# Optimization experiments

Measured on AMD Instinct MI355X. Metric: run time of the kernel, lower is better.

The kernel has to match this reference:

```python
import jax, jax.numpy as jnp
import numpy as np

D, H = 256, 4            # model dim, num heads
HD = D // H              # head dim (even, needed by rotate_half)
B, N, M, NS = 2, 6, 512, 512  # batch, views, t keypoints, s keypoints
EPS = 1e-5


def _linear(x, w, b):
    return x @ w + b


def _ln(x, g, b):
    mu = x.mean(-1, keepdims=True)
    var = ((x - mu) ** 2).mean(-1, keepdims=True)
    return (x - mu) * jax.lax.rsqrt(var + EPS) * g + b


def _ffn(x, f1w, f1b, lng, lnb, f2w, f2b):
    # Linear(2d,2d) -> LayerNorm -> exact GELU -> Linear(2d,d)
    h = jax.nn.gelu(_ln(_linear(x, f1w, f1b), lng, lnb), approximate=False)
    return _linear(h, f2w, f2b)


def _rotate_half(x):
    # pairs (x0,x1) -> (-x1, x0), interleaved
    return jnp.stack((-x[..., 1::2], x[..., 0::2]), axis=-1).reshape(x.shape)


def _rope(freqs, t):
    return t * freqs[0] + _rotate_half(t) * freqs[1]


def _attn(q, k, v):
    sim = jnp.einsum('...id,...jd->...ij', q, k) * (q.shape[-1] ** -0.5)
    return jnp.einsum('...ij,...jd->...id', jax.nn.softmax(sim, axis=-1), v)


def _self_block(x, enc, qkv_w, qkv_b, out_w, out_b, *ffn_p):
    b, n_img, m, d = x.shape
    enc = jnp.swapaxes(enc, 2, 3)  # encoding.dim()==6 path
    qkv = _linear(x, qkv_w, qkv_b).reshape(b, n_img, m, H, HD, 3)
    qkv = jnp.swapaxes(qkv, -4, -3)  # [b,N,H,m,hd,3]
    q, k, v = qkv[..., 0], qkv[..., 1], qkv[..., 2]
    ctx = _attn(_rope(enc, q), _rope(enc, k), v)  # [b,N,H,m,hd]
    msg = _linear(jnp.swapaxes(ctx, -3, -2).reshape(b, n_img, m, d), out_w, out_b)
    return x + _ffn(jnp.concatenate([x, msg], -1), *ffn_p)


def _t2t_block(t, qkv_w, qkv_b, out_w, out_b, *ffn_p):
    t2 = jnp.swapaxes(t, 1, 2)  # [b,m,N,d]
    b, m, n_img, d = t2.shape
    qkv = _linear(t2, qkv_w, qkv_b).reshape(b, m, n_img, H, HD, 3)
    qkv = jnp.swapaxes(qkv, 3, 2)  # [b,m,H,N,hd,3]
    q, k, v = qkv[..., 0], qkv[..., 1], qkv[..., 2]
    ctx = _attn(q, k, v)  # [b,m,H,N,hd]
    msg = _linear(jnp.swapaxes(ctx, 3, 2).reshape(b, m, n_img, d), out_w, out_b)
    return jnp.swapaxes(t2 + _ffn(jnp.concatenate([t2, msg], -1), *ffn_p), 1, 2)


def _s2s_block(s, q_enc, k_enc, qkv_w, qkv_b, out_w, out_b, *ffn_p):
    b, n_img, n, d = s.shape
    qkv = _linear(s, qkv_w, qkv_b).reshape(b, n_img, n, H, HD, 3)
    qkv = jnp.swapaxes(jnp.swapaxes(qkv, -4, -3), -5, -4)  # [b,H,N,n,hd,3]
    q, k, v = qkv[..., 0], qkv[..., 1], qkv[..., 2]
    # expand queries across all views, RoPE per (i,j) view pair
    q = jnp.broadcast_to(q[:, :, None], (b, H, n_img, n_img, n, HD))
    q = _rope(q_enc, q).reshape(b, H, n_img, n_img * n, HD)
    k = _rope(k_enc, k)
    ctx = _attn(q, k, v).reshape(b, H, n_img, n_img, n, HD)
    # drop diagonal (i==j) entries exactly like boolean-mask indexing in torch
    off = np.nonzero(~np.eye(n_img, dtype=bool).ravel())[0]
    ctx = ctx.reshape(b, H, n_img * n_img, n, HD)[:, :, off]
    ctx = ctx.reshape(b, H, n_img - 1, n_img, n, HD).mean(2)  # [b,H,N,n,hd]
    ctx = jnp.swapaxes(jnp.swapaxes(ctx, 1, 2), 2, 3).reshape(b, n_img, n, d)
    msg = _linear(ctx, out_w, out_b)
    return s + _ffn(jnp.concatenate([s, msg], -1), *ffn_p)


def _cross_block(d0, d1, q_w, q_b, kv_w, kv_b, out_w, out_b, *ffn_p):
    b, n_img, m, d = d0.shape
    m1 = d1.shape[2]
    q = jnp.swapaxes(_linear(d0, q_w, q_b).reshape(b, n_img, m, H, HD), 2, 3)
    kv = jnp.swapaxes(_linear(d1, kv_w, kv_b).reshape(b, n_img, m1, H, HD, 2), 2, 3)
    ctx = _attn(q, kv[..., 0], kv[..., 1])  # [b,N,H,m,hd]
    msg = _linear(jnp.swapaxes(ctx, 2, 3).reshape(b, n_img, m, d), out_w, out_b)
    return d0 + _ffn(jnp.concatenate([d0, msg], -1), *ffn_p)


def setup_inputs() -> dict:
    key = jax.random.key(0)
    ks = iter(jax.random.split(key, 80))
    f32 = jnp.float32

    def lin(din, dout):
        return (jax.random.normal(next(ks), (din, dout), f32) * (din ** -0.5),
                jnp.zeros((dout,), f32))

    inp = {}
    inp['t_desc'] = jax.random.normal(next(ks), (B, N, M, D), f32)
    inp['s_desc'] = jax.random.normal(next(ks), (B, N, NS, D), f32)
    inp['t_encoding'] = jax.random.normal(next(ks), (2, 1, 1, N, M, HD), f32)
    inp['s_encoding'] = jax.random.normal(next(ks), (2, 1, 1, N, NS, HD), f32)
    inp['q_encoding'] = jax.random.normal(next(ks), (2, 1, 1, N, N, 1, HD), f32)
    inp['k_encoding'] = jax.random.normal(next(ks), (2, 1, 1, N, NS, HD), f32)
    for pre in ('sa', 'ss', 'tt'):
        inp[pre + '_qkv_w'], inp[pre + '_qkv_b'] = lin(D, 3 * D)
        inp[pre + '_out_w'], inp[pre + '_out_b'] = lin(D, D)
        inp[pre + '_f1_w'], inp[pre + '_f1_b'] = lin(2 * D, 2 * D)
        inp[pre + '_ln_g'] = jnp.ones((2 * D,), f32)
        inp[pre + '_ln_b'] = jnp.zeros((2 * D,), f32)
        inp[pre + '_f2_w'], inp[pre + '_f2_b'] = lin(2 * D, D)
    inp['ca_q_w'], inp['ca_q_b'] = lin(D, D)
    inp['ca_kv_w'], inp['ca_kv_b'] = lin(D, 2 * D)
    inp['ca_out_w'], inp['ca_out_b'] = lin(D, D)
    inp['ca_f1_w'], inp['ca_f1_b'] = lin(2 * D, 2 * D)
    inp['ca_ln_g'] = jnp.ones((2 * D,), f32)
    inp['ca_ln_b'] = jnp.zeros((2 * D,), f32)
    inp['ca_f2_w'], inp['ca_f2_b'] = lin(2 * D, D)
    inp['cf_w1'], inp['cf_b1'] = lin(D, D)
    inp['cf_w2'], inp['cf_b2'] = lin(D, 1)
    return inp


def reference(t_desc, s_desc, t_encoding, s_encoding, q_encoding, k_encoding,
              sa_qkv_w, sa_qkv_b, sa_out_w, sa_out_b, sa_f1_w, sa_f1_b, sa_ln_g, sa_ln_b, sa_f2_w, sa_f2_b,
              ss_qkv_w, ss_qkv_b, ss_out_w, ss_out_b, ss_f1_w, ss_f1_b, ss_ln_g, ss_ln_b, ss_f2_w, ss_f2_b,
              tt_qkv_w, tt_qkv_b, tt_out_w, tt_out_b, tt_f1_w, tt_f1_b, tt_ln_g, tt_ln_b, tt_f2_w, tt_f2_b,
              ca_q_w, ca_q_b, ca_kv_w, ca_kv_b, ca_out_w, ca_out_b, ca_f1_w, ca_f1_b, ca_ln_g, ca_ln_b, ca_f2_w, ca_f2_b,
              cf_w1, cf_b1, cf_w2, cf_b2):
    sa = (sa_qkv_w, sa_qkv_b, sa_out_w, sa_out_b, sa_f1_w, sa_f1_b, sa_ln_g, sa_ln_b, sa_f2_w, sa_f2_b)
    t = _self_block(t_desc, t_encoding, *sa)   # shared SelfBlock weights
    s = _self_block(s_desc, s_encoding, *sa)
    t = _t2t_block(t, tt_qkv_w, tt_qkv_b, tt_out_w, tt_out_b, tt_f1_w, tt_f1_b, tt_ln_g, tt_ln_b, tt_f2_w, tt_f2_b)
    s = _s2s_block(s, q_encoding, k_encoding, ss_qkv_w, ss_qkv_b, ss_out_w, ss_out_b, ss_f1_w, ss_f1_b, ss_ln_g, ss_ln_b, ss_f2_w, ss_f2_b)
    ca = (ca_q_w, ca_q_b, ca_kv_w, ca_kv_b, ca_out_w, ca_out_b, ca_f1_w, ca_f1_b, ca_ln_g, ca_ln_b, ca_f2_w, ca_f2_b)
    t2 = _cross_block(t, s, *ca)               # shared CrossBlock weights
    s2 = _cross_block(s, t, *ca)
    conf = _linear(jax.nn.relu(_linear(jax.lax.stop_gradient(s), cf_w1, cf_b1)), cf_w2, cf_b2)[..., 0]
    return t2, s2, conf
```

## Files before the change

kernel.cpp:

```cpp
#include <hip/hip_runtime.h>
#include <hip/hip_bf16.h>
#include <math.h>

constexpr int kD   = 256;
constexpr int kH   = 4;
constexpr int kHD  = 64;
constexpr int kB   = 2;
constexpr int kN   = 6;
constexpr int kM   = 512;
constexpr int kRowsH = kB*kN*kM;
constexpr int kRows  = 2*kRowsH;
constexpr int kGrpH  = kB*kN*kH;
constexpr int kGrp   = 2*kGrpH;
constexpr size_t kTOK = (size_t)kRowsH*kD;
constexpr size_t kEncSlab = (size_t)kN*kM*kHD;
constexpr size_t kQEncSlab = (size_t)kN*kN*kHD;
constexpr float kL2E = 1.4426950408889634f;

typedef unsigned short u16;
typedef __attribute__((ext_vector_type(8))) short s16x8;
typedef __attribute__((ext_vector_type(4))) float f32x4;

__device__ __forceinline__ float wred_sum(float v){
  #pragma unroll
  for (int m=32;m>0;m>>=1) v += __shfl_xor(v, m, 64);
  return v;
}
__device__ __forceinline__ u16 f2b(float x){
  union { float f; unsigned u; } a; a.f = x;
  unsigned r = a.u + 0x7fffu + ((a.u >> 16) & 1u);
  return (u16)(r >> 16);
// ... 55 lines not shown
      C[(size_t)(row0+ty*4+i)*512 + col0+tx*4+j] = acc[i][j];
}

__global__ __launch_bounds__(256) void biasfuse_k(FuseArgs fa)
{
  const int set = blockIdx.x >> 1;
  const int n = (blockIdx.x & 1)*256 + threadIdx.x;
  const float* W1 = fa.W1[set];
  const float* bo = fa.bout[set];
  float s = fa.b1[set][n];
  for (int k = 0; k < 256; ++k)
    s = fmaf(bo[k], W1[(size_t)(256+k)*512 + n], s);
  fa.b1p[set*512 + n] = s;
}

struct WtDesc { const float* W; const float* W2; u16* Wt; int K; int N; int ntiles; };
struct WtTable { WtDesc d[18]; };

__global__ __launch_bounds__(256) void wtcast_k(WtTable tab)
{
  int t = blockIdx.x, mi = 0;
  while (t >= tab.d[mi].ntiles) { t -= tab.d[mi].ntiles; ++mi; }
  const float* W = tab.d[mi].W;
  const float* W2 = tab.d[mi].W2;
  u16* Wt = tab.d[mi].Wt;
  const int K = tab.d[mi].K, N = tab.d[mi].N;
  const int ktn = K >> 5;
  const int nt = t / ktn, kt = t % ktn;
  const int n0 = nt*128, k0 = kt*32;
  u16* dst = Wt + (size_t)t*4096;
  #pragma unroll
  for (int s = 0; s < 2; ++s) {
    const int idx0 = (s*256 + (int)threadIdx.x)*8;
    const int ar = idx0 >> 5;
    const int w8 = (idx0 >> 3) & 3;
    const int sw = (ar >> 1) & 3;
    int kk = k0 + ((w8 ^ sw) << 3);
    const int n  = n0 + ar;
    const float* src = W;
    if (W2 && kk >= 256) { src = W2; kk -= 256; }
    union { u16 u[8]; s16x8 v; } o;
    #pragma unroll
    for (int e = 0; e < 8; ++e)
      o.u[e] = f2b(src[(size_t)(kk + e)*N + n]);
    *(s16x8*)(dst + idx0) = o.v;
  }
}

template<bool A1B, bool A2B, bool CB>
__global__ __launch_bounds__(256) void mmad_k(
    const void* __restrict__ A1a, const void* __restrict__ A1b,
    const void* __restrict__ A2a, const void* __restrict__ A2b, int K1,
    const u16* __restrict__ Wa, const u16* __restrict__ Wb,
    const float* __restrict__ bia, const float* __restrict__ bib,
    const float* __restrict__ bi2a, const float* __restrict__ bi2b, int Ns,
    const float* __restrict__ Ra, const float* __restrict__ Rb,
    void* __restrict__ Cp, int N, int K, int Mh, int doRelu)
{
  __shared__ u16 As[128*32];
  __shared__ u16 Bs[128*32];
  const int tid = threadIdx.x;
  const int lane = tid & 63, w = tid >> 6;
  const int gx = gridDim.x;
  const int nblk = gx * gridDim.y;
  int flat = blockIdx.y*gx + blockIdx.x;
  if (!(nblk & 7)) flat = (flat & 7)*(nblk >> 3) + (flat >> 3);
  const int bxx = flat % gx, byy = flat / gx;
  const int row0 = byy*128, col0 = bxx*128;
  const bool sec = (row0 >= Mh);
  const int lr0 = sec ? row0 - Mh : row0;
  const void* A1 = sec ? A1b : A1a;
  const void* A2 = sec ? A2b : A2a;
// ... 59 lines not shown
    }
    #pragma unroll
    for (int fn = 0; fn < 4; ++fn) {
      const int c = wc + fn*16 + (lane & 15);
      const int g = (lane >> 4) ^ ((c >> 1) & 3);
      bfv[fn] = *(const s16x8*)(&Bs[c*32 + g*8]);
    }
    #pragma unroll
    for (int fm = 0; fm < 4; ++fm)
      #pragma unroll
      for (int fn = 0; fn < 4; ++fn)
        acc[fm][fn] = __builtin_amdgcn_mfma_f32_16x16x32_bf16(af[fm], bfv[fn], acc[fm][fn], 0, 0, 0);
    __syncthreads();
  }

  #pragma unroll
  for (int fm = 0; fm < 4; ++fm) {
    const int ro = wr + fm*16 + (lane >> 4)*4;
    #pragma unroll
    for (int fn = 0; fn < 4; ++fn) {
      const int cc = col0 + wc + fn*16 + (lane & 15);
      const float bv = (cc < Ns) ? bias[cc] : bias2[cc - Ns];
      #pragma unroll
      for (int j = 0; j < 4; ++j) {
        float v = acc[fm][fn][j] + bv;
        if (R) v += R[(size_t)(lr0 + ro + j)*N + cc];
        if (doRelu) v = fmaxf(v, 0.f);
        const size_t idx = (size_t)(row0 + ro + j)*N + cc;
        if constexpr (CB) ((u16*)Cp)[idx] = f2b(v);
        else              ((float*)Cp)[idx] = v;
      }
    }
  }
}

__global__ __launch_bounds__(256) void prep_self_k(
    const u16* __restrict__ qkvU, const float* __restrict__ t_enc,
    const float* __restrict__ s_enc,
    u16* __restrict__ Qb, u16* __restrict__ Kb, u16* __restrict__ Vt)
{
  __shared__ u16 vs[64][66];
  const int g = blockIdx.x >> 3, i0 = (blockIdx.x & 7)*64;
  const int h = g & 3, bn = g >> 2;
  const float* enc = (bn < 12) ? t_enc : s_enc;
  const int n = (bn < 12 ? bn : bn - 12) % kN;
  const int c = threadIdx.x & 63, t4 = threadIdx.x >> 6;
  const float sgn = (c & 1) ? 1.f : -1.f;
  #pragma unroll 4
  for (int rr = 0; rr < 16; ++rr) {
    const int il = rr*4 + t4, i = i0 + il;
    const u16* base = qkvU + ((size_t)bn*kM + i)*768 + h*192;
    const float q = b2f(base[c*3]), k = b2f(base[c*3+1]);
    const float qp = b2f(base[(c^1)*3]), kp = b2f(base[(c^1)*3+1]);
    const size_t eo = ((size_t)(n*kM + i))*kHD + c;
    const float e0 = enc[eo], e1 = enc[kEncSlab + eo];
    Qb[((size_t)g*kM + i)*kHD + c] = f2b((q*e0 + sgn*qp*e1)*0.125f);
    Kb[((size_t)g*kM + i)*kHD + c] = f2b(k*e0 + sgn*kp*e1);
    vs[il][c] = base[c*3+2];
  }
  __syncthreads();
  #pragma unroll 4
  for (int rr = 0; rr < 16; ++rr) {
    const int cc = rr*4 + t4;
    Vt[((size_t)g*kHD + cc)*kM + i0 + c] = vs[c][cc];
  }
}

__global__ __launch_bounds__(256) void prep_s2s_k(
    const u16* __restrict__ qkvU, const float* __restrict__ kenc,
    float* __restrict__ Qs, u16* __restrict__ Kb, u16* __restrict__ Vt)
{
  __shared__ u16 vs[64][66];
  const int g = blockIdx.x >> 3, i0 = (blockIdx.x & 7)*64;
  const int view = g % kN, bh = g / kN;
  const int h = bh & 3, b = bh >> 2;
  const int c = threadIdx.x & 63, t4 = threadIdx.x >> 6;
  const float sgn = (c & 1) ? 1.f : -1.f;
  #pragma unroll 4
  for (int rr = 0; rr < 16; ++rr) {
    const int il = rr*4 + t4, i = i0 + il;
    const u16* base = qkvU + ((size_t)(kRowsH + (b*kN+view)*kM + i))*768 + h*192;
    const float k = b2f(base[c*3+1]), kp = b2f(base[(c^1)*3+1]);
    const size_t eo = ((size_t)(view*kM + i))*kHD + c;
    const float e0 = kenc[eo], e1 = kenc[kEncSlab + eo];
    Qs[((size_t)g*kM + i)*kHD + c] = b2f(base[c*3]);
    Kb[((size_t)g*kM + i)*kHD + c] = f2b(k*e0 + sgn*kp*e1);
    vs[il][c] = base[c*3+2];
  }
  __syncthreads();
  #pragma unroll 4
  for (int rr = 0; rr < 16; ++rr) {
    const int cc = rr*4 + t4;
    Vt[((size_t)g*kHD + cc)*kM + i0 + c] = vs[c][cc];
  }
}

__global__ __launch_bounds__(256) void prep_cross_k(
    const u16* __restrict__ qkvC, u16* __restrict__ Kb, u16* __restrict__ Vt)
{
  __shared__ u16 vs[64][66];
  const int g = blockIdx.x >> 3, i0 = (blockIdx.x & 7)*64;
  const int h = g & 3, bn = g >> 2;
  const int src = (bn < 12) ? bn + 12 : bn - 12;
  const int c = threadIdx.x & 63, t4 = threadIdx.x >> 6;
  #pragma unroll 4
  for (int rr = 0; rr < 16; ++rr) {
    const int il = rr*4 + t4, i = i0 + il;
    const u16* base = qkvC + ((size_t)src*kM + i)*768 + 256 + h*128;
    Kb[((size_t)g*kM + i)*kHD + c] = f2b(b2f(base[c*2]) * 0.125f);
    vs[il][c] = base[c*2+1];
  }
  __syncthreads();
  #pragma unroll 4
  for (int rr = 0; rr < 16; ++rr) {
    const int cc = rr*4 + t4;
    Vt[((size_t)g*kHD + cc)*kM + i0 + c] = vs[c][cc];
  }
}

template<int CROSSQ>
__global__ __launch_bounds__(256) void attn_mm_k(
    const u16* __restrict__ Qb, const u16* __restrict__ Kb,
    const u16* __restrict__ Vt, u16* __restrict__ ctx)
{
  const int w = threadIdx.x >> 6, lane = threadIdx.x & 63;
  const int bij = (blockIdx.x & 7)*48 + (blockIdx.x >> 3);
  const int g = bij >> 2, qblk = bij & 3;
  const int h = g & 3, bn = g >> 2;
  const int q0 = qblk*128 + w*32;
  const int qr = lane & 15, hi = lane >> 4;
  const bool subhi = (hi & 1), up = (hi >= 2);

  s16x8 qf0[2], qf1[2];
  #pragma unroll
  for (int f = 0; f < 2; ++f) {
    const u16* qp = CROSSQ
      ? Qb + ((size_t)(bn*kM + q0 + f*16 + qr))*768 + h*kHD + hi*8
      : Qb + ((size_t)g*kM + q0 + f*16 + qr)*kHD + hi*8;
    qf0[f] = *(const s16x8*)(qp);
    qf1[f] = *(const s16x8*)(qp + 32);
  }

  const u16* Kg = Kb + (size_t)g*kM*kHD;
  const u16* Vg = Vt + (size_t)g*kHD*kM;
  f32x4 acc[2][4] = {};
  float m[2] = {-1e30f, -1e30f}, l[2] = {0.f, 0.f};

  for (int kc = 0; kc < 16; ++kc) {
    const int k0 = kc*32;
    s16x8 a0[2], a1[2];
    #pragma unroll
    for (int t = 0; t < 2; ++t) {
      const u16* kp = Kg + ((size_t)(k0 + t*16 + qr))*kHD + hi*8;
      a0[t] = *(const s16x8*)(kp);
      a1[t] = *(const s16x8*)(kp + 32);
    }
    s16x8 pa[2];
    #pragma unroll
    for (int f = 0; f < 2; ++f) {
// ... 63 lines not shown
    lf += __shfl_xor(lf, 16); lf += __shfl_xor(lf, 32);
    const float li = 1.f/lf;
    const float l0 = __shfl(li, hi*4+0), l1 = __shfl(li, hi*4+1);
    const float l2 = __shfl(li, hi*4+2), l3 = __shfl(li, hi*4+3);
    #pragma unroll
    for (int db = 0; db < 4; ++db) {
      const size_t base = ((size_t)(bn*kM + q0 + f*16 + hi*4))*kD + h*kHD + db*16 + qr;
      ctx[base + 0*kD] = f2b(acc[f][db][0]*l0);
      ctx[base + 1*kD] = f2b(acc[f][db][1]*l1);
      ctx[base + 2*kD] = f2b(acc[f][db][2]*l2);
      ctx[base + 3*kD] = f2b(acc[f][db][3]*l3);
    }
  }
}

__device__ __forceinline__ void rope4(const f32x4 x, const f32x4 e0, const f32x4 e1, float o[4])
{
  o[0] = x[0]*e0[0] - x[1]*e1[0];
  o[1] = x[1]*e0[1] + x[0]*e1[1];
  o[2] = x[2]*e0[2] - x[3]*e1[2];
  o[3] = x[3]*e0[3] + x[2]*e1[3];
}

__global__ __launch_bounds__(256) void attn_s2s_k(
    const float* __restrict__ Qraw, const u16* __restrict__ Kb,
    const u16* __restrict__ Vt, const float* __restrict__ qenc,
    u16* __restrict__ ctx5)
{
  const int w = threadIdx.x >> 6, lane = threadIdx.x & 63;
  const int bij = (blockIdx.x & 7)*120 + (blockIdx.x >> 3);
  const int bh = bij / 120;
  const int rest = bij % 120;
  const int col = rest / 20;
  const int rem = rest % 20;
  const int qblk = rem / 5, split = rem % 5;
  const int q0 = qblk*128 + w*32;
  const int qr = lane & 15, hi = lane >> 4;
  const bool subhi = (hi & 1), up = (hi >= 2);

  const int e  = split*6 + col;
  const int iv = e/5;
  const int j0 = e%5;
  const int jv = j0 + (j0 >= iv ? 1 : 0);

  s16x8 qf0[2], qf1[2];
  #pragma unroll
  for (int f = 0; f < 2; ++f) {
    const float* qp = Qraw + ((size_t)(bh*kN + jv)*kM + q0 + f*16 + qr)*kHD + hi*8;
    const float* ep = qenc + ((size_t)(iv*kN + jv))*kHD + hi*8;
    union { u16 u[8]; s16x8 v; } A, B;
    float o[4];
    rope4(*(const f32x4*)(qp),   *(const f32x4*)(ep),   *(const f32x4*)(ep+kQEncSlab), o);
    #pragma unroll
    for (int j = 0; j < 4; ++j) A.u[j] = f2b(o[j]*0.125f);
    rope4(*(const f32x4*)(qp+4), *(const f32x4*)(ep+4), *(const f32x4*)(ep+kQEncSlab+4), o);
    #pragma unroll
    for (int j = 0; j < 4; ++j) A.u[4+j] = f2b(o[j]*0.125f);
    rope4(*(const f32x4*)(qp+32), *(const f32x4*)(ep+32), *(const f32x4*)(ep+kQEncSlab+32), o);
    #pragma unroll
    for (int j = 0; j < 4; ++j) B.u[j] = f2b(o[j]*0.125f);
    rope4(*(const f32x4*)(qp+36), *(const f32x4*)(ep+36), *(const f32x4*)(ep+kQEncSlab+36), o);
    #pragma unroll
    for (int j = 0; j < 4; ++j) B.u[4+j] = f2b(o[j]*0.125f);
    qf0[f] = A.v; qf1[f] = B.v;
  }

  const int g2 = bh*kN + iv;
  const u16* Kg = Kb + (size_t)g2*kM*kHD;
  const u16* Vg = Vt + (size_t)g2*kHD*kM;
  f32x4 acc[2][4] = {};
  float m[2] = {-1e30f, -1e30f}, l[2] = {0.f, 0.f};

  for (int kc = 0; kc < 16; ++kc) {
    const int k0 = kc*32;
    s16x8 a0[2], a1[2];
    #pragma unroll
    for (int t = 0; t < 2; ++t) {
      const u16* kp = Kg + ((size_t)(k0 + t*16 + qr))*kHD + hi*8;
      a0[t] = *(const s16x8*)(kp);
      a1[t] = *(const s16x8*)(kp + 32);
    }
    s16x8 pa[2];
    #pragma unroll
    for (int f = 0; f < 2; ++f) {
// ... 82 lines not shown
{
  const size_t i4 = ((size_t)blockIdx.x*256 + threadIdx.x)*4;
  float s0=0.f, s1=0.f, s2=0.f, s3=0.f;
  #pragma unroll
  for (int sp = 0; sp < 5; ++sp) {
    uint2 d = *(const uint2*)(c5 + sp*kTOK + i4);
    s0 += b2f((u16)(d.x & 0xffff)); s1 += b2f((u16)(d.x >> 16));
    s2 += b2f((u16)(d.y & 0xffff)); s3 += b2f((u16)(d.y >> 16));
  }
  union { u16 u[4]; uint2 d; } o;
  o.u[0]=f2b(s0); o.u[1]=f2b(s1); o.u[2]=f2b(s2); o.u[3]=f2b(s3);
  *(uint2*)(outU + i4) = o.d;
}

__global__ __launch_bounds__(256) void attn_t2t_k(
    const u16* __restrict__ qkvU, u16* __restrict__ ctxU)
{
  const int wid = blockIdx.x*4 + (threadIdx.x >> 6);
  const int lane = threadIdx.x & 63;
  const int m = wid & 511;
  const int t = wid >> 9;
  const int nq = t % kN;
  const int bh = t / kN;
  const int h = bh & 3, b = bh >> 2;
  const u16* pb[kN];
  #pragma unroll
  for (int nk = 0; nk < kN; ++nk)
    pb[nk] = qkvU + ((size_t)(b*kN+nk)*kM + m)*768 + h*192;
  const float qc = b2f(pb[nq][lane*3]);
  float sim[kN];
  #pragma unroll
  for (int nk = 0; nk < kN; ++nk)
    sim[nk] = wred_sum(qc * b2f(pb[nk][lane*3+1])) * 0.125f;
  float mx = sim[0];
  #pragma unroll
  for (int nk = 1; nk < kN; ++nk) mx = fmaxf(mx, sim[nk]);
  float p[kN], s = 0.f;
  #pragma unroll
  for (int nk = 0; nk < kN; ++nk) { p[nk] = expf(sim[nk]-mx); s += p[nk]; }
  const float inv = 1.f/s;
  float o = 0.f;
  #pragma unroll
  for (int nk = 0; nk < kN; ++nk) o = fmaf(p[nk], b2f(pb[nk][lane*3+2]), o);
  ctxU[((size_t)(b*kN+nq)*kM + m)*kD + h*kHD + lane] = f2b(o*inv);
}

__global__ __launch_bounds__(256) void lngelu_k(
    const float* __restrict__ x, u16* __restrict__ y,
    const float* __restrict__ g0, const float* __restrict__ b0,
    const float* __restrict__ g1, const float* __restrict__ b1, int Mh)
{
  const int row = blockIdx.x;
  const int tid = threadIdx.x;
  const float* g = (row < Mh) ? g0 : g1;
  const float* bb = (row < Mh) ? b0 : b1;
  const float* xr = x + (size_t)row*512;
  const float v0 = xr[tid], v1 = xr[tid+256];
  const int w = tid >> 6, lane = tid & 63;
// ... 35 lines not shown
  const float* s_enc  = F(3);
  const float* q_enc  = F(4);
  const float* k_enc  = F(5);

  char* base = (char*)d_ws;
  float* xts = (float*)base;
  float* xt = xts;
  float* xs = xts + kTOK;
  char* R1  = base + 2*kTOK*sizeof(float);
  char* CTX = R1 + 4*kTOK*sizeof(float);
  char* MSG = CTX + 2*kTOK*sizeof(u16);
  u16* Qb16 = (u16*)(MSG + kTOK*sizeof(float));
  u16* Kb16 = Qb16 + 2*kTOK;
  u16* Vt16 = Kb16 + 2*kTOK;
  u16* wsW  = Vt16 + 2*kTOK;
  u16*   qkvU  = (u16*)R1;
  float* hbuf  = (float*)R1;
  u16*   ctx5  = (u16*)R1;
  float* Wtmp  = (float*)R1;
  u16*   ctxU  = (u16*)CTX;
  float* Qs2s  = (float*)MSG;
  float* confb = (float*)MSG;
  u16*   yU    = (u16*)CTX;

  float* out_t2s2 = (float*)d_out;
  float* out_conf = (float*)d_out + 2*kTOK;

  WtTable tab;
  int nd = 0, total_tiles = 0;
  size_t woff = 0;
  const u16* wp[18];
  auto addw = [&](int idx, const float* W2, int K, int N){
    u16* dst = wsW + woff;
    tab.d[nd] = { F(idx), W2, dst, K, N, (N>>7)*(K>>5) };
    total_tiles += tab.d[nd].ntiles;
    wp[nd] = dst;
    woff += (size_t)K*N;
    ++nd;
    return nd-1;
  };
  const int W_SA_QKV = addw(6,  nullptr, 256, 768);
  const int W_SA_F1  = addw(10, Wtmp + 0*131072, 512, 512);
  const int W_SA_F2  = addw(14, nullptr, 512, 256);
  const int W_SS_QKV = addw(16, nullptr, 256, 768);
  const int W_SS_F1  = addw(20, Wtmp + 1*131072, 512, 512);
  const int W_SS_F2  = addw(24, nullptr, 512, 256);
  const int W_TT_QKV = addw(26, nullptr, 256, 768);
  const int W_TT_F1  = addw(30, Wtmp + 2*131072, 512, 512);
  const int W_TT_F2  = addw(34, nullptr, 512, 256);
  const int W_CA_Q   = addw(36, nullptr, 256, 256);
  const int W_CA_KV  = addw(38, nullptr, 256, 512);
  const int W_CA_F1  = addw(42, Wtmp + 3*131072, 512, 512);
  const int W_CA_F2  = addw(46, nullptr, 512, 256);
  const int W_CF_1   = addw(48, nullptr, 256, 256);
  (void)W_CA_KV;
  float* b1p = (float*)(wsW + woff);

  FuseArgs fa;
  fa.Wout[0]=F(8);  fa.Wout[1]=F(18); fa.Wout[2]=F(28); fa.Wout[3]=F(40);
  fa.W1[0]=F(10);   fa.W1[1]=F(20);   fa.W1[2]=F(30);   fa.W1[3]=F(42);
  fa.bout[0]=F(9);  fa.bout[1]=F(19); fa.bout[2]=F(29); fa.bout[3]=F(41);
  fa.b1[0]=F(11);   fa.b1[1]=F(21);   fa.b1[2]=F(31);   fa.b1[3]=F(43);
  fa.Wtmp = Wtmp; fa.b1p = b1p;
  wfuse_k<<<128, 256, 0, stream>>>(fa);
  biasfuse_k<<<8, 256, 0, stream>>>(fa);
  wtcast_k<<<total_tiles, 256, 0, stream>>>(tab);

  auto mm_f32_to_b16 = [&](const float* a1a, const float* a1b, int wa, int wb2,
                           const float* ba, const float* bb2, u16* c, int N_, int K_){
    dim3 grid(N_/128, kRows/128);
    mmad_k<false,false,true><<<grid,256,0,stream>>>(a1a, a1b, nullptr, nullptr, K_,
        wp[wa], wp[wb2], ba, bb2, ba, bb2, N_, nullptr, nullptr, c, N_, K_, kRowsH, 0);
  };
  auto mm_f1 = [&](const float* a1a, const float* a1b, const u16* a2a, const u16* a2b,
                   int wa, int wb2, const float* ba, const float* bb2, float* c){
    dim3 grid(512/128, kRows/128);
    mmad_k<false,true,false><<<grid,256,0,stream>>>(a1a, a1b, a2a, a2b, 256,
        wp[wa], wp[wb2], ba, bb2, ba, bb2, 512, nullptr, nullptr, c, 512, 512, kRowsH, 0);
  };
  auto mm_f2 = [&](const u16* a1a, const u16* a1b, int wa, int wb2,
                   const float* ba, const float* bb2,
                   const float* ra, const float* rb, float* c){
    dim3 grid(256/128, kRows/128);
    mmad_k<true,false,false><<<grid,256,0,stream>>>(a1a, a1b, nullptr, nullptr, 512,
        wp[wa], wp[wb2], ba, bb2, ba, bb2, 256, ra, rb, c, 256, 512, kRowsH, 0);
  };

  mm_f32_to_b16(t_desc, s_desc, W_SA_QKV, W_SA_QKV, F(7), F(7), qkvU, 768, 256);
  prep_self_k<<<kGrp*8, 256, 0, stream>>>(qkvU, t_enc, s_enc, Qb16, Kb16, Vt16);
  attn_mm_k<0><<<384, 256, 0, stream>>>(Qb16, Kb16, Vt16, ctxU);
  mm_f1(t_desc, s_desc, ctxU, ctxU + kTOK, W_SA_F1, W_SA_F1, b1p+0*512, b1p+0*512, hbuf);
  lngelu_k<<<kRows, 256, 0, stream>>>(hbuf, yU, F(12), F(13), F(12), F(13), kRowsH);
  mm_f2(yU, yU + (size_t)kRowsH*512, W_SA_F2, W_SA_F2, F(15), F(15), t_desc, s_desc, xts);

  mm_f32_to_b16(xt, xs, W_TT_QKV, W_SS_QKV, F(27), F(17), qkvU, 768, 256);
  prep_s2s_k<<<kGrpH*8, 256, 0, stream>>>(qkvU, k_enc, Qs2s, Kb16, Vt16);
  attn_t2t_k<<<(kB*kH*kN*kM)/4, 256, 0, stream>>>(qkvU, ctxU);
  attn_s2s_k<<<960, 256, 0, stream>>>(Qs2s, Kb16, Vt16, q_enc, ctx5);
  sum5_k<<<(int)(kTOK/1024), 256, 0, stream>>>(ctx5, ctxU + kTOK);
  mm_f1(xt, xs, ctxU, ctxU + kTOK, W_TT_F1, W_SS_F1, b1p+2*512, b1p+1*512, hbuf);
  lngelu_k<<<kRows, 256, 0, stream>>>(hbuf, yU, F(32), F(33), F(22), F(23), kRowsH);
  mm_f2(yU, yU + (size_t)kRowsH*512, W_TT_F2, W_SS_F2, F(35), F(25), xt, xs, xts);

  {
    dim3 grid(2, kRowsH/128);
    mmad_k<false,false,false><<<grid,256,0,stream>>>(xs, xs, nullptr, nullptr, 256,
        wp[W_CF_1], wp[W_CF_1], F(49), F(49), F(49), F(49), 256,
        nullptr, nullptr, confb, 256, 256, kRowsH, 1);
  }
  conf_dot_k<<<kRowsH/4, 256, 0, stream>>>(confb, F(50), F(51), out_conf);

  {
    dim3 grid(768/128, kRows/128);
    mmad_k<false,false,true><<<grid,256,0,stream>>>(xt, xs, nullptr, nullptr, 256,
        wp[W_CA_Q], wp[W_CA_Q], F(37), F(37), F(39), F(39), 256,
        nullptr, nullptr, qkvU, 768, 256, kRowsH, 0);
  }
  prep_cross_k<<<kGrp*8, 256, 0, stream>>>(qkvU, Kb16, Vt16);
  attn_mm_k<1><<<384, 256, 0, stream>>>(qkvU, Kb16, Vt16, ctxU);
  mm_f1(xt, xs, ctxU, ctxU + kTOK, W_CA_F1, W_CA_F1, b1p+3*512, b1p+3*512, hbuf);
  lngelu_k<<<kRows, 256, 0, stream>>>(hbuf, yU, F(44), F(45), F(44), F(45), kRowsH);
  mm_f2(yU, yU + (size_t)kRowsH*512, W_CA_F2, W_CA_F2, F(47), F(47), xt, xs, out_t2s2);
}
```

Baseline: 483.6 us.

## Fuse QKV projection epilogues with RoPE and head-major scatter, drop prep kernels

The QKV weight columns are permuted at cast time so each output tile groups q, k and v for a head. The GEMM epilogue then applies the bias, RoPE (exchanging the pair partner via a lane shuffle) and the scaling, and writes Q/K/V directly in per-head layouts. This removes the intermediate qkv buffer and the separate prep kernels. A small transpose kernel still builds V^T, and t2t and s2s attention now read the pre-split buffers, at the cost of scattered 2-byte stores from the GEMM epilogue.

Measured after the change: 508.2 us. 1.05x slower.

```diff
diff --git a/kernel.cpp b/kernel.cpp
--- a/kernel.cpp
+++ b/kernel.cpp
@@ -15,6 +15,7 @@
 constexpr size_t kTOK = (size_t)kRowsH*kD;
 constexpr size_t kEncSlab = (size_t)kN*kM*kHD;
 constexpr size_t kQEncSlab = (size_t)kN*kN*kHD;
+constexpr size_t kGS = (size_t)kM*kHD;
 constexpr float kL2E = 1.4426950408889634f;
 
 typedef unsigned short u16;
@@ -100,8 +101,8 @@
   fa.b1p[set*512 + n] = s;
 }
 
-struct WtDesc { const float* W; const float* W2; u16* Wt; int K; int N; int ntiles; };
-struct WtTable { WtDesc d[18]; };
+struct WtDesc { const float* W; const float* W2; u16* Wt; int K; int N; int ntiles; int perm; };
+struct WtTable { WtDesc d[16]; };
 
 __global__ __launch_bounds__(256) void wtcast_k(WtTable tab)
 {
@@ -110,7 +111,7 @@
   const float* W = tab.d[mi].W;
   const float* W2 = tab.d[mi].W2;
   u16* Wt = tab.d[mi].Wt;
-  const int K = tab.d[mi].K, N = tab.d[mi].N;
+  const int K = tab.d[mi].K, N = tab.d[mi].N, perm = tab.d[mi].perm;
   const int ktn = K >> 5;
   const int nt = t / ktn, kt = t % ktn;
   const int n0 = nt*128, k0 = kt*32;
@@ -123,17 +124,30 @@
     const int sw = (ar >> 1) & 3;
     int kk = k0 + ((w8 ^ sw) << 3);
     const int n  = n0 + ar;
+    int o = n;
+    if (perm == 1) {
+      const int hh = n / 192, rem = n % 192;
+      o = hh*192 + (rem & 63)*3 + (rem >> 6);
+    } else if (perm == 2) {
+      const int hh = n >> 7, rem = n & 127;
+      o = hh*128 + (rem & 63)*2 + (rem >> 6);
+    }
     const float* src = W;
     if (W2 && kk >= 256) { src = W2; kk -= 256; }
-    union { u16 u[8]; s16x8 v; } o;
+    union { u16 u[8]; s16x8 v; } ov;
     #pragma unroll
     for (int e = 0; e < 8; ++e)
-      o.u[e] = f2b(src[(size_t)(kk + e)*N + n]);
-    *(s16x8*)(dst + idx0) = o.v;
-  }
-}
-
-template<bool A1B, bool A2B, bool CB>
+      ov.u[e] = f2b(src[(size_t)(kk + e)*N + o]);
+    *(s16x8*)(dst + idx0) = ov.v;
+  }
+}
+
+struct EpiArgs {
+  const float* enc_t; const float* enc_s;
+  u16 *Qb, *Kb, *Vst, *Qs2s;
+};
+
+template<bool A1B, bool A2B, int EPI>
 __global__ __launch_bounds__(256) void mmad_k(
     const void* __restrict__ A1a, const void* __restrict__ A1b,
     const void* __restrict__ A2a, const void* __restrict__ A2b, int K1,
@@ -141,7 +155,7 @@
     const float* __restrict__ bia, const float* __restrict__ bib,
     const float* __restrict__ bi2a, const float* __restrict__ bi2b, int Ns,
     const float* __restrict__ Ra, const float* __restrict__ Rb,
-    void* __restrict__ Cp, int N, int K, int Mh, int doRelu)
+    float* __restrict__ Cp, int N, int K, int Mh, int doRelu, EpiArgs ea)
 {
   __shared__ u16 As[128*32];
   __shared__ u16 Bs[128*32];
@@ -231,111 +245,129 @@
     __syncthreads();
   }
 
-  #pragma unroll
-  for (int fm = 0; fm < 4; ++fm) {
-    const int ro = wr + fm*16 + (lane >> 4)*4;
-    #pragma unroll
-    for (int fn = 0; fn < 4; ++fn) {
-      const int cc = col0 + wc + fn*16 + (lane & 15);
-      const float bv = (cc < Ns) ? bias[cc] : bias2[cc - Ns];
-      #pragma unroll
-      for (int j = 0; j < 4; ++j) {
-        float v = acc[fm][fn][j] + bv;
-        if (R) v += R[(size_t)(lr0 + ro + j)*N + cc];
-        if (doRelu) v = fmaxf(v, 0.f);
-        const size_t idx = (size_t)(row0 + ro + j)*N + cc;
-        if constexpr (CB) ((u16*)Cp)[idx] = f2b(v);
-        else              ((float*)Cp)[idx] = v;
+  if constexpr (EPI == 0) {
+    #pragma unroll
+    for (int fm = 0; fm < 4; ++fm) {
+      const int ro = wr + fm*16 + (lane >> 4)*4;
+      #pragma unroll
+      for (int fn = 0; fn < 4; ++fn) {
+        const int cc = col0 + wc + fn*16 + (lane & 15);
+        const float bv = (cc < Ns) ? bias[cc] : bias2[cc - Ns];
+        #pragma unroll
+        for (int j = 0; j < 4; ++j) {
+          float v = acc[fm][fn][j] + bv;
+          if (R) v += R[(size_t)(lr0 + ro + j)*N + cc];
+          if (doRelu) v = fmaxf(v, 0.f);
+          Cp[(size_t)(row0 + ro + j)*N + cc] = v;
+        }
       }
     }
-  }
-}
-
-__global__ __launch_bounds__(256) void prep_self_k(
-    const u16* __restrict__ qkvU, const float* __restrict__ t_enc,
-    const float* __restrict__ s_enc,
-    u16* __restrict__ Qb, u16* __restrict__ Kb, u16* __restrict__ Vt)
+  } else {
+    const int bn = row0 >> 9;
+    const int ib = (row0 & 511);
+    #pragma unroll
+    for (int fm = 0; fm < 4; ++fm) {
+      const int ro = wr + fm*16 + (lane >> 4)*4;
+      #pragma unroll
+      for (int fn = 0; fn < 4; ++fn) {
+        const int cc = col0 + wc + fn*16 + (lane & 15);
+        if constexpr (EPI == 1 || EPI == 2) {
+          const int hh = cc/192, rem = cc%192;
+          const int which = rem >> 6, hd = rem & 63;
+          const float bv = bias[hh*192 + hd*3 + which];
+          const float sgn = (hd & 1) ? 1.f : -1.f;
+          #pragma unroll
+          for (int j = 0; j < 4; ++j) {
+            const int i = ib + ro + j;
+            const float vb = acc[fm][fn][j] + bv;
+            if constexpr (EPI == 1) {
+              const bool isT = (bn < 12);
+              const float* enc = isT ? ea.enc_t : ea.enc_s;
+              const int n = (isT ? bn : bn - 12) % kN;
+              const size_t base = ((size_t)(bn*4+hh)*kM + i)*kHD + hd;
+              if (which == 2) {
+                ea.Vst[base] = f2b(vb);
+              } else {
+                const float vp = __shfl_xor(vb, 1);
+                const size_t eo = ((size_t)(n*kM + i))*kHD + hd;
+                const float rv = vb*enc[eo] + sgn*vp*enc[kEncSlab + eo];
+                if (which == 0) ea.Qb[base] = f2b(rv*0.125f);
+                else            ea.Kb[base] = f2b(rv);
+              }
+            } else {
+              if (bn < 12) {
+                const size_t base = ((size_t)(bn*4+hh)*kM + i)*kHD + hd;
+                if (which == 0)      ea.Qb [base] = f2b(vb);
+                else if (which == 1) ea.Kb [48*kGS + base] = f2b(vb);
+                else                 ea.Vst[48*kGS + base] = f2b(vb);
+              } else {
+                const int bns = bn - 12;
+                const int b = bns / kN, view = bns % kN;
+                const int g2 = (b*4 + hh)*kN + view;
+                const size_t base = ((size_t)g2*kM + i)*kHD + hd;
+                if (which == 0) {
+                  ea.Qs2s[base] = f2b(vb*0.125f);
+                } else if (which == 1) {
+                  const float vp = __shfl_xor(vb, 1);
+                  const size_t eo = ((size_t)(view*kM + i))*kHD + hd;
+                  const float rv = vb*ea.enc_s[eo] + sgn*vp*ea.enc_s[kEncSlab + eo];
+                  ea.Kb[base] = f2b(rv);
+                } else {
+                  ea.Qb[48*kGS + base] = f2b(vb);
+                }
+              }
+            }
+          }
+        } else {
+          if (cc < 256) {
+            const int hh = cc >> 6, hd = cc & 63;
+            const float bv = bias[cc];
+            #pragma unroll
+            for (int j = 0; j < 4; ++j) {
+              const int i = ib + ro + j;
+              const float vb = acc[fm][fn][j] + bv;
+              ea.Qb[((size_t)(bn*4+hh)*kM + i)*kHD + hd] = f2b(vb*0.125f);
+            }
+          } else {
+            const int p = cc - 256;
+            const int hh = p >> 7, rem = p & 127;
+            const int which = rem >> 6, hd = rem & 63;
+            const float bv = bias2[hh*128 + hd*2 + which];
+            const int bnsw = (bn < 12) ? bn + 12 : bn - 12;
+            #pragma unroll
+            for (int j = 0; j < 4; ++j) {
+              const int i = ib + ro + j;
+              const float vb = acc[fm][fn][j] + bv;
+              const size_t base = ((size_t)(bnsw*4+hh)*kM + i)*kHD + hd;
+              if (which == 0) ea.Kb [base] = f2b(vb);
+              else            ea.Vst[base] = f2b(vb);
+            }
+          }
+        }
+      }
+    }
+  }
+}
+
+__global__ __launch_bounds__(256) void vtrans_k(const u16* __restrict__ src,
+                                               u16* __restrict__ dst)
 {
   __shared__ u16 vs[64][66];
   const int g = blockIdx.x >> 3, i0 = (blockIdx.x & 7)*64;
-  const int h = g & 3, bn = g >> 2;
-  const float* enc = (bn < 12) ? t_enc : s_enc;
-  const int n = (bn < 12 ? bn : bn - 12) % kN;
   const int c = threadIdx.x & 63, t4 = threadIdx.x >> 6;
-  const float sgn = (c & 1) ? 1.f : -1.f;
   #pragma unroll 4
   for (int rr = 0; rr < 16; ++rr) {
-    const int il = rr*4 + t4, i = i0 + il;
-    const u16* base = qkvU + ((size_t)bn*kM + i)*768 + h*192;
-    const float q = b2f(base[c*3]), k = b2f(base[c*3+1]);
-    const float qp = b2f(base[(c^1)*3]), kp = b2f(base[(c^1)*3+1]);
-    const size_t eo = ((size_t)(n*kM + i))*kHD + c;
-    const float e0 = enc[eo], e1 = enc[kEncSlab + eo];
-    Qb[((size_t)g*kM + i)*kHD + c] = f2b((q*e0 + sgn*qp*e1)*0.125f);
-    Kb[((size_t)g*kM + i)*kHD + c] = f2b(k*e0 + sgn*kp*e1);
-    vs[il][c] = base[c*3+2];
+    const int il = rr*4 + t4;
+    vs[il][c] = src[((size_t)g*kM + i0 + il)*kHD + c];
   }
   __syncthreads();
   #pragma unroll 4
   for (int rr = 0; rr < 16; ++rr) {
     const int cc = rr*4 + t4;
-    Vt[((size_t)g*kHD + cc)*kM + i0 + c] = vs[c][cc];
-  }
-}
-
-__global__ __launch_bounds__(256) void prep_s2s_k(
-    const u16* __restrict__ qkvU, const float* __restrict__ kenc,
-    float* __restrict__ Qs, u16* __restrict__ Kb, u16* __restrict__ Vt)
-{
-  __shared__ u16 vs[64][66];
-  const int g = blockIdx.x >> 3, i0 = (blockIdx.x & 7)*64;
-  const int view = g % kN, bh = g / kN;
-  const int h = bh & 3, b = bh >> 2;
-  const int c = threadIdx.x & 63, t4 = threadIdx.x >> 6;
-  const float sgn = (c & 1) ? 1.f : -1.f;
-  #pragma unroll 4
-  for (int rr = 0; rr < 16; ++rr) {
-    const int il = rr*4 + t4, i = i0 + il;
-    const u16* base = qkvU + ((size_t)(kRowsH + (b*kN+view)*kM + i))*768 + h*192;
-    const float k = b2f(base[c*3+1]), kp = b2f(base[(c^1)*3+1]);
-    const size_t eo = ((size_t)(view*kM + i))*kHD + c;
-    const float e0 = kenc[eo], e1 = kenc[kEncSlab + eo];
-    Qs[((size_t)g*kM + i)*kHD + c] = b2f(base[c*3]);
-    Kb[((size_t)g*kM + i)*kHD + c] = f2b(k*e0 + sgn*kp*e1);
-    vs[il][c] = base[c*3+2];
-  }
-  __syncthreads();
-  #pragma unroll 4
-  for (int rr = 0; rr < 16; ++rr) {
-    const int cc = rr*4 + t4;
-    Vt[((size_t)g*kHD + cc)*kM + i0 + c] = vs[c][cc];
-  }
-}
-
-__global__ __launch_bounds__(256) void prep_cross_k(
-    const u16* __restrict__ qkvC, u16* __restrict__ Kb, u16* __restrict__ Vt)
-{
-  __shared__ u16 vs[64][66];
-  const int g = blockIdx.x >> 3, i0 = (blockIdx.x & 7)*64;
-  const int h = g & 3, bn = g >> 2;
-  const int src = (bn < 12) ? bn + 12 : bn - 12;
-  const int c = threadIdx.x & 63, t4 = threadIdx.x >> 6;
-  #pragma unroll 4
-  for (int rr = 0; rr < 16; ++rr) {
-    const int il = rr*4 + t4, i = i0 + il;
-    const u16* base = qkvC + ((size_t)src*kM + i)*768 + 256 + h*128;
-    Kb[((size_t)g*kM + i)*kHD + c] = f2b(b2f(base[c*2]) * 0.125f);
-    vs[il][c] = base[c*2+1];
-  }
-  __syncthreads();
-  #pragma unroll 4
-  for (int rr = 0; rr < 16; ++rr) {
-    const int cc = rr*4 + t4;
-    Vt[((size_t)g*kHD + cc)*kM + i0 + c] = vs[c][cc];
-  }
-}
-
-template<int CROSSQ>
+    dst[((size_t)g*kHD + cc)*kM + i0 + c] = vs[c][cc];
+  }
+}
+
 __global__ __launch_bounds__(256) void attn_mm_k(
     const u16* __restrict__ Qb, const u16* __restrict__ Kb,
     const u16* __restrict__ Vt, u16* __restrict__ ctx)
@@ -351,15 +383,13 @@
   s16x8 qf0[2], qf1[2];
   #pragma unroll
   for (int f = 0; f < 2; ++f) {
-    const u16* qp = CROSSQ
-      ? Qb + ((size_t)(bn*kM + q0 + f*16 + qr))*768 + h*kHD + hi*8
-      : Qb + ((size_t)g*kM + q0 + f*16 + qr)*kHD + hi*8;
+    const u16* qp = Qb + ((size_t)g*kM + q0 + f*16 + qr)*kHD + hi*8;
     qf0[f] = *(const s16x8*)(qp);
     qf1[f] = *(const s16x8*)(qp + 32);
   }
 
-  const u16* Kg = Kb + (size_t)g*kM*kHD;
-  const u16* Vg = Vt + (size_t)g*kHD*kM;
+  const u16* Kg = Kb + (size_t)g*kGS;
+  const u16* Vg = Vt + (size_t)g*kGS;
   f32x4 acc[2][4] = {};
   float m[2] = {-1e30f, -1e30f}, l[2] = {0.f, 0.f};
 
@@ -453,16 +483,20 @@
   }
 }
 
-__device__ __forceinline__ void rope4(const f32x4 x, const f32x4 e0, const f32x4 e1, float o[4])
-{
-  o[0] = x[0]*e0[0] - x[1]*e1[0];
-  o[1] = x[1]*e0[1] + x[0]*e1[1];
-  o[2] = x[2]*e0[2] - x[3]*e1[2];
-  o[3] = x[3]*e0[3] + x[2]*e1[3];
+__device__ __forceinline__ s16x8 ropeq(const u16* qp, const float* ep)
+{
+  union { u16 u[8]; s16x8 v; } o;
+  #pragma unroll
+  for (int u2 = 0; u2 < 8; u2 += 2) {
+    const float a = b2f(qp[u2]), b = b2f(qp[u2+1]);
+    o.u[u2]   = f2b(a*ep[u2]   - b*ep[kQEncSlab + u2]);
+    o.u[u2+1] = f2b(b*ep[u2+1] + a*ep[kQEncSlab + u2+1]);
+  }
+  return o.v;
 }
 
 __global__ __launch_bounds__(256) void attn_s2s_k(
-    const float* __restrict__ Qraw, const u16* __restrict__ Kb,
+    const u16* __restrict__ Qs2sU, const u16* __restrict__ Kb,
     const u16* __restrict__ Vt, const float* __restrict__ qenc,
     u16* __restrict__ ctx5)
 {
@@ -483,30 +517,17 @@
   const int jv = j0 + (j0 >= iv ? 1 : 0);
 
   s16x8 qf0[2], qf1[2];
+  const float* ep = qenc + ((size_t)(iv*kN + jv))*kHD + hi*8;
   #pragma unroll
   for (int f = 0; f < 2; ++f) {
-    const float* qp = Qraw + ((size_t)(bh*kN + jv)*kM + q0 + f*16 + qr)*kHD + hi*8;
-    const float* ep = qenc + ((size_t)(iv*kN + jv))*kHD + hi*8;
-    union { u16 u[8]; s16x8 v; } A, B;
-    float o[4];
-    rope4(*(const f32x4*)(qp),   *(const f32x4*)(ep),   *(const f32x4*)(ep+kQEncSlab), o);
-    #pragma unroll
-    for (int j = 0; j < 4; ++j) A.u[j] = f2b(o[j]*0.125f);
-    rope4(*(const f32x4*)(qp+4), *(const f32x4*)(ep+4), *(const f32x4*)(ep+kQEncSlab+4), o);
-    #pragma unroll
-    for (int j = 0; j < 4; ++j) A.u[4+j] = f2b(o[j]*0.125f);
-    rope4(*(const f32x4*)(qp+32), *(const f32x4*)(ep+32), *(const f32x4*)(ep+kQEncSlab+32), o);
-    #pragma unroll
-    for (int j = 0; j < 4; ++j) B.u[j] = f2b(o[j]*0.125f);
-    rope4(*(const f32x4*)(qp+36), *(const f32x4*)(ep+36), *(const f32x4*)(ep+kQEncSlab+36), o);
-    #pragma unroll
-    for (int j = 0; j < 4; ++j) B.u[4+j] = f2b(o[j]*0.125f);
-    qf0[f] = A.v; qf1[f] = B.v;
+    const u16* qp = Qs2sU + ((size_t)(bh*kN + jv)*kM + q0 + f*16 + qr)*kHD + hi*8;
+    qf0[f] = ropeq(qp, ep);
+    qf1[f] = ropeq(qp + 32, ep + 32);
   }
 
   const int g2 = bh*kN + iv;
-  const u16* Kg = Kb + (size_t)g2*kM*kHD;
-  const u16* Vg = Vt + (size_t)g2*kHD*kM;
+  const u16* Kg = Kb + (size_t)g2*kGS;
+  const u16* Vg = Vt + (size_t)g2*kGS;
   f32x4 acc[2][4] = {};
   float m[2] = {-1e30f, -1e30f}, l[2] = {0.f, 0.f};
 
@@ -619,7 +640,8 @@
 }
 
 __global__ __launch_bounds__(256) void attn_t2t_k(
-    const u16* __restrict__ qkvU, u16* __restrict__ ctxU)
+    const u16* __restrict__ Qp, const u16* __restrict__ Kp,
+    const u16* __restrict__ Vp, u16* __restrict__ ctxU)
 {
   const int wid = blockIdx.x*4 + (threadIdx.x >> 6);
   const int lane = threadIdx.x & 63;
@@ -628,15 +650,13 @@
   const int nq = t % kN;
   const int bh = t / kN;
   const int h = bh & 3, b = bh >> 2;
-  const u16* pb[kN];
-  #pragma unroll
-  for (int nk = 0; nk < kN; ++nk)
-    pb[nk] = qkvU + ((size_t)(b*kN+nk)*kM + m)*768 + h*192;
-  const float qc = b2f(pb[nq][lane*3]);
+  const float qc = b2f(Qp[((size_t)((b*kN+nq)*4+h)*kM + m)*kHD + lane]);
   float sim[kN];
   #pragma unroll
-  for (int nk = 0; nk < kN; ++nk)
-    sim[nk] = wred_sum(qc * b2f(pb[nk][lane*3+1])) * 0.125f;
+  for (int nk = 0; nk < kN; ++nk) {
+    const size_t gb = ((size_t)((b*kN+nk)*4+h)*kM + m)*kHD + lane;
+    sim[nk] = wred_sum(qc * b2f(Kp[gb])) * 0.125f;
+  }
   float mx = sim[0];
   #pragma unroll
   for (int nk = 1; nk < kN; ++nk) mx = fmaxf(mx, sim[nk]);
@@ -646,7 +666,10 @@
   const float inv = 1.f/s;
   float o = 0.f;
   #pragma unroll
-  for (int nk = 0; nk < kN; ++nk) o = fmaf(p[nk], b2f(pb[nk][lane*3+2]), o);
+  for (int nk = 0; nk < kN; ++nk) {
+    const size_t gb = ((size_t)((b*kN+nk)*4+h)*kM + m)*kHD + lane;
+    o = fmaf(p[nk], b2f(Vp[gb]), o);
+  }
   ctxU[((size_t)(b*kN+nq)*kM + m)*kD + h*kHD + lane] = f2b(o*inv);
 }
 
@@ -712,12 +735,12 @@
   u16* Kb16 = Qb16 + 2*kTOK;
   u16* Vt16 = Kb16 + 2*kTOK;
   u16* wsW  = Vt16 + 2*kTOK;
-  u16*   qkvU  = (u16*)R1;
   float* hbuf  = (float*)R1;
   u16*   ctx5  = (u16*)R1;
   float* Wtmp  = (float*)R1;
   u16*   ctxU  = (u16*)CTX;
-  float* Qs2s  = (float*)MSG;
+  u16*   vstg  = (u16*)MSG;
+  u16*   Qs2sU = (u16*)MSG;
   float* confb = (float*)MSG;
   u16*   yU    = (u16*)CTX;
 
@@ -727,30 +750,30 @@
   WtTable tab;
   int nd = 0, total_tiles = 0;
   size_t woff = 0;
-  const u16* wp[18];
-  auto addw = [&](int idx, const float* W2, int K, int N){
+  const u16* wp[16];
+  auto addw = [&](int idx, const float* W2, int K, int N, int perm){
     u16* dst = wsW + woff;
-    tab.d[nd] = { F(idx), W2, dst, K, N, (N>>7)*(K>>5) };
+    tab.d[nd] = { F(idx), W2, dst, K, N, (N>>7)*(K>>5), perm };
     total_tiles += tab.d[nd].ntiles;
     wp[nd] = dst;
     woff += (size_t)K*N;
     ++nd;
     return nd-1;
   };
-  const int W_SA_QKV = addw(6,  nullptr, 256, 768);
-  const int W_SA_F1  = addw(10, Wtmp + 0*131072, 512, 512);
-  const int W_SA_F2  = addw(14, nullptr, 512, 256);
-  const int W_SS_QKV = addw(16, nullptr, 256, 768);
-  const int W_SS_F1  = addw(20, Wtmp + 1*131072, 512, 512);
-  const int W_SS_F2  = addw(24, nullptr, 512, 256);
-  const int W_TT_QKV = addw(26, nullptr, 256, 768);
-  const int W_TT_F1  = addw(30, Wtmp + 2*131072, 512, 512);
-  const int W_TT_F2  = addw(34, nullptr, 512, 256);
-  const int W_CA_Q   = addw(36, nullptr, 256, 256);
-  const int W_CA_KV  = addw(38, nullptr, 256, 512);
-  const int W_CA_F1  = addw(42, Wtmp + 3*131072, 512, 512);
-  const int W_CA_F2  = addw(46, nullptr, 512, 256);
-  const int W_CF_1   = addw(48, nullptr, 256, 256);
+  const int W_SA_QKV = addw(6,  nullptr, 256, 768, 1);
+  const int W_SA_F1  = addw(10, Wtmp + 0*131072, 512, 512, 0);
+  const int W_SA_F2  = addw(14, nullptr, 512, 256, 0);
+  const int W_SS_QKV = addw(16, nullptr, 256, 768, 1);
+  const int W_SS_F1  = addw(20, Wtmp + 1*131072, 512, 512, 0);
+  const int W_SS_F2  = addw(24, nullptr, 512, 256, 0);
+  const int W_TT_QKV = addw(26, nullptr, 256, 768, 1);
+  const int W_TT_F1  = addw(30, Wtmp + 2*131072, 512, 512, 0);
+  const int W_TT_F2  = addw(34, nullptr, 512, 256, 0);
+  const int W_CA_Q   = addw(36, nullptr, 256, 256, 0);
+  const int W_CA_KV  = addw(38, nullptr, 256, 512, 2);
+  const int W_CA_F1  = addw(42, Wtmp + 3*131072, 512, 512, 0);
+  const int W_CA_F2  = addw(46, nullptr, 512, 256, 0);
+  const int W_CF_1   = addw(48, nullptr, 256, 256, 0);
   (void)W_CA_KV;
   float* b1p = (float*)(wsW + woff);
 
@@ -764,37 +787,44 @@
   biasfuse_k<<<8, 256, 0, stream>>>(fa);
   wtcast_k<<<total_tiles, 256, 0, stream>>>(tab);
 
-  auto mm_f32_to_b16 = [&](const float* a1a, const float* a1b, int wa, int wb2,
-                           const float* ba, const float* bb2, u16* c, int N_, int K_){
-    dim3 grid(N_/128, kRows/128);
-    mmad_k<false,false,true><<<grid,256,0,stream>>>(a1a, a1b, nullptr, nullptr, K_,
-        wp[wa], wp[wb2], ba, bb2, ba, bb2, N_, nullptr, nullptr, c, N_, K_, kRowsH, 0);
-  };
+  const EpiArgs ea0 = {};
   auto mm_f1 = [&](const float* a1a, const float* a1b, const u16* a2a, const u16* a2b,
                    int wa, int wb2, const float* ba, const float* bb2, float* c){
     dim3 grid(512/128, kRows/128);
-    mmad_k<false,true,false><<<grid,256,0,stream>>>(a1a, a1b, a2a, a2b, 256,
-        wp[wa], wp[wb2], ba, bb2, ba, bb2, 512, nullptr, nullptr, c, 512, 512, kRowsH, 0);
+    mmad_k<false,true,0><<<grid,256,0,stream>>>(a1a, a1b, a2a, a2b, 256,
+        wp[wa], wp[wb2], ba, bb2, ba, bb2, 512, nullptr, nullptr, c, 512, 512, kRowsH, 0, ea0);
   };
   auto mm_f2 = [&](const u16* a1a, const u16* a1b, int wa, int wb2,
                    const float* ba, const float* bb2,
                    const float* ra, const float* rb, float* c){
     dim3 grid(256/128, kRows/128);
-    mmad_k<true,false,false><<<grid,256,0,stream>>>(a1a, a1b, nullptr, nullptr, 512,
-        wp[wa], wp[wb2], ba, bb2, ba, bb2, 256, ra, rb, c, 256, 512, kRowsH, 0);
+    mmad_k<true,false,0><<<grid,256,0,stream>>>(a1a, a1b, nullptr, nullptr, 512,
+        wp[wa], wp[wb2], ba, bb2, ba, bb2, 256, ra, rb, c, 256, 512, kRowsH, 0, ea0);
   };
 
-  mm_f32_to_b16(t_desc, s_desc, W_SA_QKV, W_SA_QKV, F(7), F(7), qkvU, 768, 256);
-  prep_self_k<<<kGrp*8, 256, 0, stream>>>(qkvU, t_enc, s_enc, Qb16, Kb16, Vt16);
-  attn_mm_k<0><<<384, 256, 0, stream>>>(Qb16, Kb16, Vt16, ctxU);
+  {
+    EpiArgs ea = { t_enc, s_enc, Qb16, Kb16, vstg, nullptr };
+    dim3 grid(6, 96);
+    mmad_k<false,false,1><<<grid,256,0,stream>>>(t_desc, s_desc, nullptr, nullptr, 256,
+        wp[W_SA_QKV], wp[W_SA_QKV], F(7), F(7), F(7), F(7), 768,
+        nullptr, nullptr, nullptr, 768, 256, kRowsH, 0, ea);
+  }
+  vtrans_k<<<96*8, 256, 0, stream>>>(vstg, Vt16);
+  attn_mm_k<<<384, 256, 0, stream>>>(Qb16, Kb16, Vt16, ctxU);
   mm_f1(t_desc, s_desc, ctxU, ctxU + kTOK, W_SA_F1, W_SA_F1, b1p+0*512, b1p+0*512, hbuf);
   lngelu_k<<<kRows, 256, 0, stream>>>(hbuf, yU, F(12), F(13), F(12), F(13), kRowsH);
   mm_f2(yU, yU + (size_t)kRowsH*512, W_SA_F2, W_SA_F2, F(15), F(15), t_desc, s_desc, xts);
 
-  mm_f32_to_b16(xt, xs, W_TT_QKV, W_SS_QKV, F(27), F(17), qkvU, 768, 256);
-  prep_s2s_k<<<kGrpH*8, 256, 0, stream>>>(qkvU, k_enc, Qs2s, Kb16, Vt16);
-  attn_t2t_k<<<(kB*kH*kN*kM)/4, 256, 0, stream>>>(qkvU, ctxU);
-  attn_s2s_k<<<960, 256, 0, stream>>>(Qs2s, Kb16, Vt16, q_enc, ctx5);
+  {
+    EpiArgs ea = { nullptr, k_enc, Qb16, Kb16, Vt16, Qs2sU };
+    dim3 grid(6, 96);
+    mmad_k<false,false,2><<<grid,256,0,stream>>>(xt, xs, nullptr, nullptr, 256,
+        wp[W_TT_QKV], wp[W_SS_QKV], F(27), F(17), F(27), F(17), 768,
+        nullptr, nullptr, nullptr, 768, 256, kRowsH, 0, ea);
+  }
+  vtrans_k<<<48*8, 256, 0, stream>>>(Qb16 + 48*kGS, Vt16);
+  attn_t2t_k<<<(kB*kH*kN*kM)/4, 256, 0, stream>>>(Qb16, Kb16 + 48*kGS, Vt16 + 48*kGS, ctxU);
+  attn_s2s_k<<<960, 256, 0, stream>>>(Qs2sU, Kb16, Vt16, q_enc, ctx5);
   sum5_k<<<(int)(kTOK/1024), 256, 0, stream>>>(ctx5, ctxU + kTOK);
   mm_f1(xt, xs, ctxU, ctxU + kTOK, W_TT_F1, W_SS_F1, b1p+2*512, b1p+1*512, hbuf);
   lngelu_k<<<kRows, 256, 0, stream>>>(hbuf, yU, F(32), F(33), F(22), F(23), kRowsH);
@@ -802,20 +832,21 @@
 
   {
     dim3 grid(2, kRowsH/128);
-    mmad_k<false,false,false><<<grid,256,0,stream>>>(xs, xs, nullptr, nullptr, 256,
+    mmad_k<false,false,0><<<grid,256,0,stream>>>(xs, xs, nullptr, nullptr, 256,
         wp[W_CF_1], wp[W_CF_1], F(49), F(49), F(49), F(49), 256,
-        nullptr, nullptr, confb, 256, 256, kRowsH, 1);
+        nullptr, nullptr, confb, 256, 256, kRowsH, 1, ea0);
   }
   conf_dot_k<<<kRowsH/4, 256, 0, stream>>>(confb, F(50), F(51), out_conf);
 
   {
-    dim3 grid(768/128, kRows/128);
-    mmad_k<false,false,true><<<grid,256,0,stream>>>(xt, xs, nullptr, nullptr, 256,
+    EpiArgs ea = { nullptr, nullptr, Qb16, Kb16, vstg, nullptr };
+    dim3 grid(6, 96);
+    mmad_k<false,false,3><<<grid,256,0,stream>>>(xt, xs, nullptr, nullptr, 256,
         wp[W_CA_Q], wp[W_CA_Q], F(37), F(37), F(39), F(39), 256,
-        nullptr, nullptr, qkvU, 768, 256, kRowsH, 0);
-  }
-  prep_cross_k<<<kGrp*8, 256, 0, stream>>>(qkvU, Kb16, Vt16);
-  attn_mm_k<1><<<384, 256, 0, stream>>>(qkvU, Kb16, Vt16, ctxU);
+        nullptr, nullptr, nullptr, 768, 256, kRowsH, 0, ea);
+  }
+  vtrans_k<<<96*8, 256, 0, stream>>>(vstg, Vt16);
+  attn_mm_k<<<384, 256, 0, stream>>>(Qb16, Kb16, Vt16, ctxU);
   mm_f1(xt, xs, ctxU, ctxU + kTOK, W_CA_F1, W_CA_F1, b1p+3*512, b1p+3*512, hbuf);
   lngelu_k<<<kRows, 256, 0, stream>>>(hbuf, yU, F(44), F(45), F(44), F(45), kRowsH);
   mm_f2(yU, yU + (size_t)kRowsH*512, W_CA_F2, W_CA_F2, F(47), F(47), xt, xs, out_t2s2);
```
